# Performance work log

Measured on AMD Instinct MI355X. Metric: run time of the kernel, lower is better.

Reference implementation:

```python
import jax, jax.numpy as jnp
import numpy as np

IN_FEATURES = 512
OUT_FEATURES = 512
GRID_MIN = -2.0
GRID_MAX = 2.0
NUM_GRIDS = 8
SPLINE_SCALE = 0.1
BATCH = 16384


def setup_inputs() -> dict:
    key = jax.random.key(0)
    kx, kw = jax.random.split(key)
    x = jax.random.normal(kx, (BATCH, IN_FEATURES), dtype=jnp.float32)
    grid = jnp.linspace(GRID_MIN, GRID_MAX, NUM_GRIDS, dtype=jnp.float32)
    spline_weight = (
        jax.random.normal(kw, (IN_FEATURES * NUM_GRIDS, OUT_FEATURES), dtype=jnp.float32)
        * SPLINE_SCALE
    )
    return {"x": x, "grid": grid, "spline_weight": spline_weight}


def reference(x, grid, spline_weight):
    # denominator h = (grid_max - grid_min) / (num_grids - 1)
    h = (GRID_MAX - GRID_MIN) / (NUM_GRIDS - 1)
    # basis: [B, in_features, num_grids]
    basis = jnp.exp(-jnp.square((x[..., None] - grid) / h))
    # flatten to [B, in_features * num_grids] and GEMM
    return basis.reshape(basis.shape[0], -1) @ spline_weight
```

## Files before the change

kernel.cpp:

```cpp
#include <hip/hip_runtime.h>
#include <hip/hip_bf16.h>

#define BATCH 16384
#define IN_F 512
#define OUT_F 512
#define NG 8
#define KTOT (IN_F * NG)

#define SH    2.1019642153762872f
#define SSTEP 1.2011224087864498f
#define BC0N  4.2039284307525745f

typedef __attribute__((ext_vector_type(8))) short short8;
typedef __attribute__((ext_vector_type(4))) float f32x4;
typedef __attribute__((ext_vector_type(2))) float f32x2;
typedef __attribute__((ext_vector_type(4))) unsigned int u32x4;
typedef __attribute__((ext_vector_type(2))) unsigned int u32x2;

__device__ __forceinline__ unsigned fbits(float f) {
    union { float f; unsigned u; } v; v.f = f; return v.u;
}
__device__ __forceinline__ unsigned short f2bf(float f) {
    return (unsigned short)((fbits(f) + 0x8000u) >> 16);
}
__device__ __forceinline__ unsigned pack2bf(float lo, float hi) {
    unsigned a = (fbits(lo) + 0x8000u) >> 16;
    unsigned b = (fbits(hi) + 0x8000u) & 0xFFFF0000u;
    return a | b;
}

__global__ void wt_convert(const float* __restrict__ W, unsigned short* __restrict__ Wt) {
    __shared__ float tile[32][33];
    const int bx = blockIdx.x;
    const int by = blockIdx.y;
    const int tx = threadIdx.x & 31;
    const int ty = threadIdx.x >> 5;
#pragma unroll
    for (int i = 0; i < 4; ++i) {
        int kl = ty + i * 8;
        tile[kl][tx] = W[(size_t)(bx * 32 + kl) * OUT_F + by * 32 + tx];
    }
    __syncthreads();
#pragma unroll
    for (int i = 0; i < 4; ++i) {
        int nl = ty + i * 8;
        Wt[(size_t)(by * 32 + nl) * KTOT + bx * 32 + tx] = f2bf(tile[tx][nl]);
    }
}

#define BM2 64
#define BN2 256
#define BK2 64

__global__ __launch_bounds__(256, 2) void gauss_gemm2(
        const float* __restrict__ X, const unsigned short* __restrict__ Wt,
        float* __restrict__ Out) {
    __shared__ __align__(16) unsigned short sA[BM2 * BK2];
    __shared__ __align__(16) unsigned short sB[BN2 * BK2];

    const int tid  = threadIdx.x;
    const int lane = tid & 63;
    const int wave = tid >> 6;
    const int rb = blockIdx.x >> 1;
    const int cb = blockIdx.x & 1;
    const int m0 = rb * BM2;
    const int n0 = cb * BN2;
    const int l15 = lane & 15;
    const int lq  = lane >> 4;

    const int arow = tid >> 2;
    const int axp  = tid & 3;
    const float* xp = X + (size_t)(m0 + arow) * IN_F + 2 * axp;
    unsigned short* a0p = sA + arow * BK2 + ((((axp << 1)    ) ^ (arow & 7)) << 3);
    unsigned short* a1p = sA + arow * BK2 + ((((axp << 1) | 1) ^ (arow & 7)) << 3);

    const int brow = lane >> 3;
    const int bch  = (lane & 7) ^ brow;
    const unsigned short* bsrc =
        Wt + (size_t)(n0 + wave * 64 + brow) * KTOT + bch * 8;

    f32x4 acc[4][4];
#pragma unroll
    for (int i = 0; i < 4; ++i)
#pragma unroll
        for (int j = 0; j < 4; ++j)
            acc[i][j] = (f32x4){0.f, 0.f, 0.f, 0.f};

    for (int kt = 0; kt < KTOT / BK2; ++kt) {
#pragma unroll
        for (int p = 0; p < 8; ++p) {
            __builtin_amdgcn_global_load_lds(
                (const __attribute__((address_space(1))) unsigned int*)
                    (const void*)(bsrc + (size_t)p * 8 * KTOT + kt * BK2),
                (__attribute__((address_space(3))) unsigned int*)
                    (void*)(sB + (wave * 64 + p * 8) * BK2),
                16, 0, 0);
        }

        const f32x2 xv = *(const f32x2*)(xp + kt * 8);
#pragma unroll
        for (int h = 0; h < 2; ++h) {
            const float xs = (h ? xv.y : xv.x) * SH;
            u32x4 pk;
#pragma unroll
            for (int g = 0; g < 8; g += 2) {
                float t0 = xs + (BC0N - g * SSTEP);
                float t1 = xs + (BC0N - (g + 1) * SSTEP);
                unsigned u0 = fbits(__builtin_amdgcn_exp2f(-t0 * t0)) + 0x8000u;
                unsigned u1 = fbits(__builtin_amdgcn_exp2f(-t1 * t1)) + 0x8000u;
                pk[g >> 1] = __builtin_amdgcn_perm(u1, u0, 0x07060302u);
            }
            *(u32x4*)(h ? a1p : a0p) = pk;
        }

        __syncthreads();

#pragma unroll
        for (int kk = 0; kk < 2; ++kk) {
            const int koff = ((((kk << 2) + lq) ^ (l15 & 7)) << 3);
            short8 af[4], bfv[4];
#pragma unroll
            for (int i = 0; i < 4; ++i)
                af[i] = *(const short8*)(sA + (i * 16 + l15) * BK2 + koff);
#pragma unroll
            for (int j = 0; j < 4; ++j)
                bfv[j] = *(const short8*)(sB + (wave * 64 + j * 16 + l15) * BK2 + koff);
#pragma unroll
            for (int i = 0; i < 4; ++i)
#pragma unroll
                for (int j = 0; j < 4; ++j)
                    acc[i][j] = __builtin_amdgcn_mfma_f32_16x16x32_bf16(af[i], bfv[j], acc[i][j], 0, 0, 0);
        }

        __syncthreads();
    }

#pragma unroll
    for (int i = 0; i < 4; ++i) {
        const int r0 = m0 + i * 16 + lq * 4;
#pragma unroll
        for (int j = 0; j < 4; ++j) {
            const int c = n0 + wave * 64 + j * 16 + l15;
#pragma unroll
            for (int e = 0; e < 4; ++e)
                Out[(size_t)(r0 + e) * OUT_F + c] = acc[i][j][e];
        }
    }
}

#define BM 128
#define BN 128
#define BK 64
#define LDA 72
#define LDB 72

__global__ __launch_bounds__(256, 2) void gauss_gemm_fb(
        const float* __restrict__ X, const float* __restrict__ W,
        float* __restrict__ Out) {
    __shared__ __align__(16) unsigned short sA[BM * LDA];
    __shared__ __align__(16) unsigned short sB[BN * LDB];

    const int tid  = threadIdx.x;
    const int lane = tid & 63;
    const int wave = tid >> 6;
    const int rb = blockIdx.x >> 2;
    const int cb = blockIdx.x & 3;
    const int m0 = rb * BM;
    const int n0 = cb * BN;
    const int wr = (wave >> 1) * 64;
    const int wc = (wave & 1) * 64;
    const int l15 = lane & 15;
    const int lq  = lane >> 4;

    f32x4 acc[4][4];
#pragma unroll
    for (int i = 0; i < 4; ++i)
#pragma unroll
        for (int j = 0; j < 4; ++j)
            acc[i][j] = (f32x4){0.f, 0.f, 0.f, 0.f};

    const int arow = tid & 127;
    const int axq  = tid >> 7;

    for (int kt = 0; kt < KTOT / BK; ++kt) {
        const int k0  = kt * BK;
        const int xc0 = kt * (BK / NG);

        const f32x4 xv = *(const f32x4*)(X + (size_t)(m0 + arow) * IN_F + xc0 + 4 * axq);
        unsigned short* sArow = sA + arow * LDA + axq * 32;
#pragma unroll
        for (int j = 0; j < 4; ++j) {
            const float xs = xv[j] * SH;
            u32x4 pk;
#pragma unroll
            for (int g = 0; g < 8; g += 2) {
                float t0 = xs + (BC0N - g * SSTEP);
                float t1 = xs + (BC0N - (g + 1) * SSTEP);
                unsigned u0 = fbits(__builtin_amdgcn_exp2f(-t0 * t0)) + 0x8000u;
                unsigned u1 = fbits(__builtin_amdgcn_exp2f(-t1 * t1)) + 0x8000u;
                pk[g >> 1] = __builtin_amdgcn_perm(u1, u0, 0x07060302u);
            }
            *(u32x4*)(sArow + j * 8) = pk;
        }

#pragma unroll
        for (int p = 0; p < 8; ++p) {
            int id = p * 256 + tid;
            int n  = id & 127;
            int k4 = id >> 7;
            const float* wp = W + (size_t)(k0 + k4 * 4) * OUT_F + n0 + n;
            u32x2 v;
            v[0] = pack2bf(wp[0], wp[OUT_F]);
            v[1] = pack2bf(wp[2 * OUT_F], wp[3 * OUT_F]);
            *(u32x2*)(sB + n * LDB + k4 * 4) = v;
        }

        __syncthreads();

#pragma unroll
        for (int kk = 0; kk < BK; kk += 32) {
            short8 af[4], bfv[4];
#pragma unroll
            for (int i = 0; i < 4; ++i)
                af[i] = *(const short8*)(sA + (wr + i * 16 + l15) * LDA + kk + lq * 8);
#pragma unroll
            for (int i = 0; i < 4; ++i)
                bfv[i] = *(const short8*)(sB + (wc + i * 16 + l15) * LDB + kk + lq * 8);
#pragma unroll
            for (int i = 0; i < 4; ++i)
#pragma unroll
                for (int j = 0; j < 4; ++j)
                    acc[i][j] = __builtin_amdgcn_mfma_f32_16x16x32_bf16(af[i], bfv[j], acc[i][j], 0, 0, 0);
        }

        __syncthreads();
    }

#pragma unroll
    for (int i = 0; i < 4; ++i) {
        const int r0 = m0 + wr + i * 16 + lq * 4;
#pragma unroll
        for (int j = 0; j < 4; ++j) {
            const int c = n0 + wc + j * 16 + l15;
#pragma unroll
            for (int e = 0; e < 4; ++e)
                Out[(size_t)(r0 + e) * OUT_F + c] = acc[i][j][e];
        }
    }
}

extern "C" void kernel_launch(void* const* d_in, const int* in_sizes, int n_in,
                              void* d_out, int out_size, void* d_ws, size_t ws_size,
                              hipStream_t stream) {
    (void)in_sizes; (void)n_in; (void)out_size;
    const float* X = (const float*)d_in[0];
    const float* W = (const float*)d_in[2];
    float* Out = (float*)d_out;

    const size_t wt_bytes = (size_t)KTOT * OUT_F * sizeof(unsigned short);
    if (ws_size >= wt_bytes) {
        unsigned short* Wt = (unsigned short*)d_ws;
        wt_convert<<<dim3(KTOT / 32, OUT_F / 32), 256, 0, stream>>>(W, Wt);
        gauss_gemm2<<<dim3((BATCH / BM2) * (OUT_F / BN2)), 256, 0, stream>>>(X, Wt, Out);
    } else {
        gauss_gemm_fb<<<dim3((BATCH / BM) * (OUT_F / BN)), 256, 0, stream>>>(X, W, Out);
    }
}
```

Baseline: 173.7 us.

## Double-buffer LDS tiles in Gaussian-basis GEMM and simplify weight conversion

The main GEMM kernel now uses two LDS buffers for A and B. The async global-to-LDS copy of the next B tile and the Gaussian basis computation of the next A tile overlap with the MFMA work on the current tile, and only one barrier runs per iteration. X values are prefetched two iterations ahead. The weight-conversion kernel drops its shared-memory transpose and instead has each thread read 8 strided fp32 values and write a packed 16-byte bf16 chunk. The cost is doubled LDS usage (80 KB per block), which may limit occupancy below the two blocks per CU requested by the launch bounds, plus higher register pressure.

```diff
diff --git a/kernel.cpp b/kernel.cpp
--- a/kernel.cpp
+++ b/kernel.cpp
@@ -20,9 +20,6 @@
 __device__ __forceinline__ unsigned fbits(float f) {
     union { float f; unsigned u; } v; v.f = f; return v.u;
 }
-__device__ __forceinline__ unsigned short f2bf(float f) {
-    return (unsigned short)((fbits(f) + 0x8000u) >> 16);
-}
 __device__ __forceinline__ unsigned pack2bf(float lo, float hi) {
     unsigned a = (fbits(lo) + 0x8000u) >> 16;
     unsigned b = (fbits(hi) + 0x8000u) & 0xFFFF0000u;
@@ -30,33 +27,34 @@
 }
 
 __global__ void wt_convert(const float* __restrict__ W, unsigned short* __restrict__ Wt) {
-    __shared__ float tile[32][33];
-    const int bx = blockIdx.x;
-    const int by = blockIdx.y;
-    const int tx = threadIdx.x & 31;
-    const int ty = threadIdx.x >> 5;
-#pragma unroll
-    for (int i = 0; i < 4; ++i) {
-        int kl = ty + i * 8;
-        tile[kl][tx] = W[(size_t)(bx * 32 + kl) * OUT_F + by * 32 + tx];
-    }
-    __syncthreads();
-#pragma unroll
-    for (int i = 0; i < 4; ++i) {
-        int nl = ty + i * 8;
-        Wt[(size_t)(by * 32 + nl) * KTOT + bx * 32 + tx] = f2bf(tile[tx][nl]);
-    }
+    const int gid  = blockIdx.x * 4 + (threadIdx.x >> 6);
+    const int lane = threadIdx.x & 63;
+    const int kw = gid & 511;
+    const int nw = gid >> 9;
+    const int n  = nw * 64 + lane;
+    const int k0 = kw * 8;
+    float v[8];
+#pragma unroll
+    for (int j = 0; j < 8; ++j)
+        v[j] = W[(size_t)(k0 + j) * OUT_F + n];
+    u32x4 pk;
+#pragma unroll
+    for (int j = 0; j < 4; ++j)
+        pk[j] = pack2bf(v[2 * j], v[2 * j + 1]);
+    *(u32x4*)(Wt + (size_t)n * KTOT + k0) = pk;
 }
 
 #define BM2 64
 #define BN2 256
 #define BK2 64
-
-__global__ __launch_bounds__(256, 2) void gauss_gemm2(
+#define ABUF (BM2 * BK2)
+#define BBUF (BN2 * BK2)
+
+__global__ __launch_bounds__(256, 2) void gauss_gemm3(
         const float* __restrict__ X, const unsigned short* __restrict__ Wt,
         float* __restrict__ Out) {
-    __shared__ __align__(16) unsigned short sA[BM2 * BK2];
-    __shared__ __align__(16) unsigned short sB[BN2 * BK2];
+    __shared__ __align__(16) unsigned short sA[2 * ABUF];
+    __shared__ __align__(16) unsigned short sB[2 * BBUF];
 
     const int tid  = threadIdx.x;
     const int lane = tid & 63;
@@ -71,8 +69,8 @@
     const int arow = tid >> 2;
     const int axp  = tid & 3;
     const float* xp = X + (size_t)(m0 + arow) * IN_F + 2 * axp;
-    unsigned short* a0p = sA + arow * BK2 + ((((axp << 1)    ) ^ (arow & 7)) << 3);
-    unsigned short* a1p = sA + arow * BK2 + ((((axp << 1) | 1) ^ (arow & 7)) << 3);
+    const int aoff0 = arow * BK2 + ((((axp << 1)    ) ^ (arow & 7)) << 3);
+    const int aoff1 = arow * BK2 + ((((axp << 1) | 1) ^ (arow & 7)) << 3);
 
     const int brow = lane >> 3;
     const int bch  = (lane & 7) ^ brow;
@@ -86,18 +84,20 @@
         for (int j = 0; j < 4; ++j)
             acc[i][j] = (f32x4){0.f, 0.f, 0.f, 0.f};
 
-    for (int kt = 0; kt < KTOT / BK2; ++kt) {
+    auto stageB = [&](int kt, int buf) {
 #pragma unroll
         for (int p = 0; p < 8; ++p) {
             __builtin_amdgcn_global_load_lds(
                 (const __attribute__((address_space(1))) unsigned int*)
-                    (const void*)(bsrc + (size_t)p * 8 * KTOT + kt * BK2),
+                    (const void*)(bsrc + (size_t)p * 8 * KTOT + (size_t)kt * BK2),
                 (__attribute__((address_space(3))) unsigned int*)
-                    (void*)(sB + (wave * 64 + p * 8) * BK2),
+                    (void*)(sB + buf * BBUF + (wave * 64 + p * 8) * BK2),
                 16, 0, 0);
         }
-
-        const f32x2 xv = *(const f32x2*)(xp + kt * 8);
+    };
+
+    auto stageA = [&](f32x2 xv, int buf) {
+        unsigned short* base = sA + buf * ABUF;
 #pragma unroll
         for (int h = 0; h < 2; ++h) {
             const float xs = (h ? xv.y : xv.x) * SH;
@@ -110,29 +110,69 @@
                 unsigned u1 = fbits(__builtin_amdgcn_exp2f(-t1 * t1)) + 0x8000u;
                 pk[g >> 1] = __builtin_amdgcn_perm(u1, u0, 0x07060302u);
             }
-            *(u32x4*)(h ? a1p : a0p) = pk;
-        }
-
+            *(u32x4*)(base + (h ? aoff1 : aoff0)) = pk;
+        }
+    };
+
+    stageB(0, 0);
+    f32x2 xv = *(const f32x2*)(xp);
+    stageA(xv, 0);
+    f32x2 xnext = *(const f32x2*)(xp + 8);
+    __syncthreads();
+
+    for (int kt = 0; kt < KTOT / BK2 - 1; ++kt) {
+        const int cur = kt & 1, nxt = cur ^ 1;
+
+        f32x2 xpf;
+        if (kt < KTOT / BK2 - 2)
+            xpf = *(const f32x2*)(xp + (size_t)(kt + 2) * 8);
+
+        stageB(kt + 1, nxt);
+
+        short8 af[2][4], bfv[2][4];
+#pragma unroll
+        for (int kk = 0; kk < 2; ++kk) {
+            const int koff = ((((kk << 2) + lq) ^ (l15 & 7)) << 3);
+#pragma unroll
+            for (int i = 0; i < 4; ++i)
+                af[kk][i] = *(const short8*)(sA + cur * ABUF + (i * 16 + l15) * BK2 + koff);
+#pragma unroll
+            for (int j = 0; j < 4; ++j)
+                bfv[kk][j] = *(const short8*)(sB + cur * BBUF + (wave * 64 + j * 16 + l15) * BK2 + koff);
+        }
+
+        stageA(xnext, nxt);
+
+#pragma unroll
+        for (int kk = 0; kk < 2; ++kk)
+#pragma unroll
+            for (int i = 0; i < 4; ++i)
+#pragma unroll
+                for (int j = 0; j < 4; ++j)
+                    acc[i][j] = __builtin_amdgcn_mfma_f32_16x16x32_bf16(af[kk][i], bfv[kk][j], acc[i][j], 0, 0, 0);
+
+        xnext = xpf;
         __syncthreads();
-
+    }
+
+    {
+        const int cur = (KTOT / BK2 - 1) & 1;
 #pragma unroll
         for (int kk = 0; kk < 2; ++kk) {
             const int koff = ((((kk << 2) + lq) ^ (l15 & 7)) << 3);
             short8 af[4], bfv[4];
 #pragma unroll
             for (int i = 0; i < 4; ++i)
-                af[i] = *(const short8*)(sA + (i * 16 + l15) * BK2 + koff);
+                af[i] = *(const short8*)(sA + cur * ABUF + (i * 16 + l15) * BK2 + koff);
 #pragma unroll
             for (int j = 0; j < 4; ++j)
-                bfv[j] = *(const short8*)(sB + (wave * 64 + j * 16 + l15) * BK2 + koff);
+                bfv[j] = *(const short8*)(sB + cur * BBUF + (wave * 64 + j * 16 + l15) * BK2 + koff);
 #pragma unroll
             for (int i = 0; i < 4; ++i)
 #pragma unroll
                 for (int j = 0; j < 4; ++j)
                     acc[i][j] = __builtin_amdgcn_mfma_f32_16x16x32_bf16(af[i], bfv[j], acc[i][j], 0, 0, 0);
         }
-
-        __syncthreads();
     }
 
 #pragma unroll
@@ -260,8 +300,8 @@
     const size_t wt_bytes = (size_t)KTOT * OUT_F * sizeof(unsigned short);
     if (ws_size >= wt_bytes) {
         unsigned short* Wt = (unsigned short*)d_ws;
-        wt_convert<<<dim3(KTOT / 32, OUT_F / 32), 256, 0, stream>>>(W, Wt);
-        gauss_gemm2<<<dim3((BATCH / BM2) * (OUT_F / BN2)), 256, 0, stream>>>(X, Wt, Out);
+        wt_convert<<<dim3(KTOT * OUT_F / (8 * 64 * 4)), 256, 0, stream>>>(W, Wt);
+        gauss_gemm3<<<dim3((BATCH / BM2) * (OUT_F / BN2)), 256, 0, stream>>>(X, Wt, Out);
     } else {
         gauss_gemm_fb<<<dim3((BATCH / BM) * (OUT_F / BN)), 256, 0, stream>>>(X, W, Out);
     }
```

Measured after the change: 171.1 us. Within noise of the previous version (-1.5%).
